# Kernel tuning notes

Measured on AMD Instinct MI355X. Metric: run time of the kernel, lower is better.

## Reference

```python
import jax, jax.numpy as jnp
import numpy as np

ALPHA = 0.1
EPS = 1e-10

def setup_inputs() -> dict:
    key = jax.random.key(0)
    k1, k2 = jax.random.split(key)
    x = jax.random.normal(k1, (64, 8192, 128), dtype=jnp.float32)   # [B, N, D]
    pv = jax.random.uniform(k2, (64, 128), dtype=jnp.float32)        # [M, D] prototypes (torch.rand init)
    return {"x": x, "pv": pv}

def _cdist(x, pv):
    # Euclidean pairwise distance via GEMM form: [B,N,D] x [M,D] -> [B,N,M]
    x2 = jnp.sum(x * x, axis=-1, keepdims=True)          # [B,N,1]
    p2 = jnp.sum(pv * pv, axis=-1)                        # [M]
    xp = jnp.einsum('bnd,md->bnm', x, pv)                 # [B,N,M]
    return jnp.sqrt(jnp.maximum(x2 + p2 - 2.0 * xp, 0.0))

def reference(x, pv):
    dist = _cdist(x, pv)                                  # [B,N,M]
    min_dist = jnp.min(dist, axis=1)                      # [B,M] closest patch per prototype
    min_pos = jnp.argmin(dist, axis=1)                    # [B,M]
    # pick, per batch, the patch position of the globally closest prototype (no-grad in original)
    idx = jnp.argmin(min_dist, axis=1)                    # [B]
    min_pos = min_pos[jnp.arange(min_pos.shape[0]), idx]  # [B]
    max_sim = jnp.exp(EPS - ALPHA * min_dist)             # [B,M]
    return (max_sim, min_pos)
```

## Files before the change

kernel.cpp:

```cpp
#include <hip/hip_runtime.h>
#include <cfloat>
#include <cmath>

#define B_ 64
#define N_ 8192
#define D_ 128
#define M_ 64
#define ROWS 256
#define KD 32
#define NKD (D_ / KD)
#define CHUNKS (N_ / ROWS)
#define ALPHA_ 0.1f
#define EPS_ 1e-10f

__global__ __launch_bounds__(256, 2)
void protomin_kernel(const float* __restrict__ x, const float* __restrict__ pv,
                     float* __restrict__ wsv, int* __restrict__ wsa) {
    __shared__ union U {
        float ps[D_][M_];
        struct R { float rv[M_][33]; int ra[M_][33]; } red;
    } u;
    __shared__ float xs[KD][ROWS];
    __shared__ float x2s[ROWS];
    __shared__ float p2s[M_];

    const int tid   = threadIdx.x;
    const int bc    = blockIdx.x;
    const int b     = bc / CHUNKS;
    const int chunk = bc % CHUNKS;
    const int rowbase = chunk * ROWS;

    const int tm8  = tid & 7;
    const int trow = tid >> 3;
    const int m0   = tm8 * 8;
    const int r0   = trow * 8;

#pragma unroll
    for (int p = 0; p < 8; ++p) {
        int li = p * 1024 + tid * 4;
        int m  = li >> 7;
        int d4 = li & 127;
        float4 v = *reinterpret_cast<const float4*>(pv + m * D_ + d4);
        u.ps[d4 + 0][m] = v.x;
        u.ps[d4 + 1][m] = v.y;
        u.ps[d4 + 2][m] = v.z;
        u.ps[d4 + 3][m] = v.w;
    }
    __syncthreads();

    if (tid < M_) {
        float s = 0.f;
#pragma unroll 8
        for (int d = 0; d < D_; ++d) { float v = u.ps[d][tid]; s = fmaf(v, v, s); }
        p2s[tid] = s;
    }

    float acc[8][8];
#pragma unroll
    for (int i = 0; i < 8; ++i)
#pragma unroll
        for (int j = 0; j < 8; ++j) acc[i][j] = 0.f;
    float x2r = 0.f;

    const float* xbase = x + ((size_t)b * N_ + rowbase) * D_;

    for (int kd = 0; kd < NKD; ++kd) {
        __syncthreads();
#pragma unroll
        for (int p = 0; p < 8; ++p) {
            int li = p * 1024 + tid * 4;
            int r  = li >> 5;
            int dd = li & 31;
            float4 v = *reinterpret_cast<const float4*>(
                xbase + (size_t)r * D_ + kd * KD + dd);
            int rb = r >> 3, rj = r & 7;
            float vv[4] = {v.x, v.y, v.z, v.w};
#pragma unroll
            for (int i = 0; i < 4; ++i) {
                int d = dd + i;
                xs[d][(((rb ^ ((d >> 2) & 7)) << 3) | rj)] = vv[i];
            }
        }
        __syncthreads();

        {
            int rb = tid >> 3, rj = tid & 7;
#pragma unroll 8
            for (int d = 0; d < KD; ++d) {
                float v = xs[d][(((rb ^ ((d >> 2) & 7)) << 3) | rj)];
                x2r = fmaf(v, v, x2r);
            }
        }

        const int dbase = kd * KD;
#pragma unroll 4
        for (int d = 0; d < KD; ++d) {
            int sb = ((trow ^ ((d >> 2) & 7)) << 3);
            float4 xa = *reinterpret_cast<const float4*>(&xs[d][sb]);
            float4 xb = *reinterpret_cast<const float4*>(&xs[d][sb + 4]);
            float4 pa = *reinterpret_cast<const float4*>(&u.ps[dbase + d][m0]);
            float4 pb = *reinterpret_cast<const float4*>(&u.ps[dbase + d][m0 + 4]);
            float xv[8] = {xa.x, xa.y, xa.z, xa.w, xb.x, xb.y, xb.z, xb.w};
            float pw[8] = {pa.x, pa.y, pa.z, pa.w, pb.x, pb.y, pb.z, pb.w};
#pragma unroll
            for (int i = 0; i < 8; ++i)
#pragma unroll
                for (int j = 0; j < 8; ++j)
                    acc[i][j] = fmaf(xv[i], pw[j], acc[i][j]);
        }
    }

    __syncthreads();
    x2s[tid] = x2r;
    __syncthreads();

    float4 xa2 = *reinterpret_cast<const float4*>(&x2s[r0]);
    float4 xb2 = *reinterpret_cast<const float4*>(&x2s[r0 + 4]);
    float x2v[8] = {xa2.x, xa2.y, xa2.z, xa2.w, xb2.x, xb2.y, xb2.z, xb2.w};
    float4 p2a = *reinterpret_cast<const float4*>(&p2s[m0]);
    float4 p2b = *reinterpret_cast<const float4*>(&p2s[m0 + 4]);
    float p2v[8] = {p2a.x, p2a.y, p2a.z, p2a.w, p2b.x, p2b.y, p2b.z, p2b.w};

#pragma unroll
    for (int j = 0; j < 8; ++j) {
        float bv = FLT_MAX; int ba = 0;
        float p2j = p2v[j];
#pragma unroll
        for (int i = 0; i < 8; ++i) {
            float d2 = fmaf(-2.f, acc[i][j], x2v[i] + p2j);
            if (d2 < bv) { bv = d2; ba = rowbase + r0 + i; }
        }
        u.red.rv[m0 + j][trow] = bv;
        u.red.ra[m0 + j][trow] = ba;
    }
    __syncthreads();

    if (tid < M_) {
        float bv = FLT_MAX; int ba = 0;
        for (int k = 0; k < 32; ++k) {
            float v = u.red.rv[tid][k];
            if (v < bv) { bv = v; ba = u.red.ra[tid][k]; }
        }
        wsv[(size_t)bc * M_ + tid] = bv;
        wsa[(size_t)bc * M_ + tid] = ba;
    }
}

__global__ void finalize_kernel(const float* __restrict__ wsv,
                                const int* __restrict__ wsa,
                                float* __restrict__ out) {
    const int b = blockIdx.x;
    const int m = threadIdx.x;
    float bv = FLT_MAX; int ba = 0;
    for (int c = 0; c < CHUNKS; ++c) {
        size_t idx = ((size_t)b * CHUNKS + c) * M_ + m;
        float v = wsv[idx];
        if (v < bv) { bv = v; ba = wsa[idx]; }
    }
    float dist = sqrtf(fmaxf(bv, 0.f));
    out[b * M_ + m] = expf(EPS_ - ALPHA_ * dist);

    __shared__ float sv[M_];
    __shared__ int   sa[M_];
    sv[m] = dist; sa[m] = ba;
    __syncthreads();
    if (m == 0) {
        float best = FLT_MAX; int bp = 0;
        for (int k = 0; k < M_; ++k) {
            if (sv[k] < best) { best = sv[k]; bp = sa[k]; }
        }
        out[B_ * M_ + b] = (float)bp;
    }
}

extern "C" void kernel_launch(void* const* d_in, const int* in_sizes, int n_in,
                              void* d_out, int out_size, void* d_ws, size_t ws_size,
                              hipStream_t stream) {
    const float* x  = (const float*)d_in[0];
    const float* pv = (const float*)d_in[1];
    float* out = (float*)d_out;

    float* wsv = (float*)d_ws;
    int*   wsa = (int*)((char*)d_ws + (size_t)B_ * CHUNKS * M_ * sizeof(float));

    hipLaunchKernelGGL(protomin_kernel, dim3(B_ * CHUNKS), dim3(256), 0, stream,
                       x, pv, wsv, wsa);
    hipLaunchKernelGGL(finalize_kernel, dim3(B_), dim3(M_), 0, stream,
                       wsv, wsa, out);
}
```

Baseline: 438.4 us.

## Rewrite distance GEMM with split-bf16 MFMA and double-buffered register prefetch

```diff
diff --git a/kernel.cpp b/kernel.cpp
--- a/kernel.cpp
+++ b/kernel.cpp
@@ -6,170 +6,210 @@
 #define N_ 8192
 #define D_ 128
 #define M_ 64
-#define ROWS 256
-#define KD 32
-#define NKD (D_ / KD)
-#define CHUNKS (N_ / ROWS)
+#define CROWS 64
+#define NCHUNK 4
+#define BROWS (CROWS*NCHUNK)
+#define NBLK (N_/BROWS)
 #define ALPHA_ 0.1f
 #define EPS_ 1e-10f
 
+typedef __attribute__((ext_vector_type(4))) float f32x4;
+typedef __attribute__((ext_vector_type(8))) short bf16x8;
+typedef __attribute__((ext_vector_type(4))) short s16x4;
+
+static __device__ __forceinline__ short f2bf(float f) {
+    unsigned u = __float_as_uint(f);
+    u += 0x7fff + ((u >> 16) & 1);
+    return (short)(u >> 16);
+}
+static __device__ __forceinline__ float bf2f(short s) {
+    return __uint_as_float(((unsigned)(unsigned short)s) << 16);
+}
+
 __global__ __launch_bounds__(256, 2)
-void protomin_kernel(const float* __restrict__ x, const float* __restrict__ pv,
-                     float* __restrict__ wsv, int* __restrict__ wsa) {
-    __shared__ union U {
-        float ps[D_][M_];
-        struct R { float rv[M_][33]; int ra[M_][33]; } red;
-    } u;
-    __shared__ float xs[KD][ROWS];
-    __shared__ float x2s[ROWS];
-    __shared__ float p2s[M_];
-
-    const int tid   = threadIdx.x;
-    const int bc    = blockIdx.x;
-    const int b     = bc / CHUNKS;
-    const int chunk = bc % CHUNKS;
-    const int rowbase = chunk * ROWS;
-
-    const int tm8  = tid & 7;
-    const int trow = tid >> 3;
-    const int m0   = tm8 * 8;
-    const int r0   = trow * 8;
-
-#pragma unroll
-    for (int p = 0; p < 8; ++p) {
-        int li = p * 1024 + tid * 4;
-        int m  = li >> 7;
-        int d4 = li & 127;
-        float4 v = *reinterpret_cast<const float4*>(pv + m * D_ + d4);
-        u.ps[d4 + 0][m] = v.x;
-        u.ps[d4 + 1][m] = v.y;
-        u.ps[d4 + 2][m] = v.z;
-        u.ps[d4 + 3][m] = v.w;
-    }
+void protomin_mfma(const float* __restrict__ x, const float* __restrict__ pv,
+                   float* __restrict__ wsv, int* __restrict__ wsa) {
+    __shared__ short xhi[2][CROWS * D_];
+    __shared__ short xlo[2][CROWS * D_];
+    __shared__ float x2s[2][CROWS];
+    __shared__ float redv[4][M_];
+    __shared__ int   redp[4][M_];
+
+    const int tid = threadIdx.x;
+    const int w   = tid >> 6;
+    const int l   = tid & 63;
+    const int lm  = l & 15, lg = l >> 4;
+    const int bid = blockIdx.x;
+    const int b   = bid >> 5;
+    const int nbase = (bid & 31) * BROWS;
+
+    const float* xblk = x + ((size_t)b * N_ + nbase) * D_;
+
+    f32x4 nv[8];
+    {
+        const f32x4* src = (const f32x4*)xblk;
+#pragma unroll
+        for (int i = 0; i < 8; ++i) nv[i] = src[(w * 8 + i) * 64 + l];
+    }
+
+    bf16x8 Bh[4][4], Bl[4][4];
+#pragma unroll
+    for (int mt = 0; mt < 4; ++mt) {
+#pragma unroll
+        for (int kt = 0; kt < 4; ++kt) {
+            const float* p = pv + (mt * 16 + lm) * D_ + kt * 32 + lg * 8;
+            f32x4 p0 = *(const f32x4*)p;
+            f32x4 p1 = *(const f32x4*)(p + 4);
+#pragma unroll
+            for (int j = 0; j < 4; ++j) {
+                short h = f2bf(p0[j]);
+                Bh[mt][kt][j] = h;
+                Bl[mt][kt][j] = f2bf(p0[j] - bf2f(h));
+            }
+#pragma unroll
+            for (int j = 0; j < 4; ++j) {
+                short h = f2bf(p1[j]);
+                Bh[mt][kt][4 + j] = h;
+                Bl[mt][kt][4 + j] = f2bf(p1[j] - bf2f(h));
+            }
+        }
+    }
+
+    auto stage = [&](int buf) {
+#pragma unroll
+        for (int i = 0; i < 8; ++i) {
+            int seg = w * 8 + i;
+            int row = seg * 2 + (l >> 5);
+            int ks  = (l & 31) * 4;
+            f32x4 v = nv[i];
+            float s = v[0] * v[0];
+            s = fmaf(v[1], v[1], s); s = fmaf(v[2], v[2], s); s = fmaf(v[3], v[3], s);
+            s += __shfl_xor(s, 1);  s += __shfl_xor(s, 2);  s += __shfl_xor(s, 4);
+            s += __shfl_xor(s, 8);  s += __shfl_xor(s, 16);
+            if ((l & 31) == 0) x2s[buf][row] = s;
+            s16x4 hv, lv;
+#pragma unroll
+            for (int j = 0; j < 4; ++j) {
+                short h = f2bf(v[j]);
+                hv[j] = h;
+                lv[j] = f2bf(v[j] - bf2f(h));
+            }
+            int sidx = row * D_ + (ks ^ ((row & 7) << 3));
+            *(s16x4*)&xhi[buf][sidx] = hv;
+            *(s16x4*)&xlo[buf][sidx] = lv;
+        }
+    };
+
+    float bv[4]; int bp[4];
+#pragma unroll
+    for (int mt = 0; mt < 4; ++mt) { bv[mt] = FLT_MAX; bp[mt] = 0; }
+
+    stage(0);
     __syncthreads();
 
+    for (int c = 0; c < NCHUNK; ++c) {
+        const int cur = c & 1;
+        if (c + 1 < NCHUNK) {
+            const f32x4* src = (const f32x4*)(xblk + (size_t)(c + 1) * CROWS * D_);
+#pragma unroll
+            for (int i = 0; i < 8; ++i) nv[i] = src[(w * 8 + i) * 64 + l];
+        }
+
+        f32x4 acc[4] = {};
+        const int arow  = w * 16 + lm;
+        const int abase = arow * D_;
+        const int aswz  = (arow & 7) << 3;
+#pragma unroll
+        for (int kt = 0; kt < 4; ++kt) {
+            int koff = (kt * 32 + lg * 8) ^ aswz;
+            bf16x8 ah = *(const bf16x8*)&xhi[cur][abase + koff];
+            bf16x8 al = *(const bf16x8*)&xlo[cur][abase + koff];
+#pragma unroll
+            for (int mt = 0; mt < 4; ++mt) {
+                acc[mt] = __builtin_amdgcn_mfma_f32_16x16x32_bf16(ah, Bh[mt][kt], acc[mt], 0, 0, 0);
+                acc[mt] = __builtin_amdgcn_mfma_f32_16x16x32_bf16(al, Bh[mt][kt], acc[mt], 0, 0, 0);
+                acc[mt] = __builtin_amdgcn_mfma_f32_16x16x32_bf16(ah, Bl[mt][kt], acc[mt], 0, 0, 0);
+                acc[mt] = __builtin_amdgcn_mfma_f32_16x16x32_bf16(al, Bl[mt][kt], acc[mt], 0, 0, 0);
+            }
+        }
+
+        float x2v[4];
+        const int rbase = w * 16 + lg * 4;
+#pragma unroll
+        for (int r = 0; r < 4; ++r) x2v[r] = x2s[cur][rbase + r];
+        const int npos0 = nbase + c * CROWS + rbase;
+#pragma unroll
+        for (int mt = 0; mt < 4; ++mt) {
+#pragma unroll
+            for (int r = 0; r < 4; ++r) {
+                float cand = fmaf(-2.f, acc[mt][r], x2v[r]);
+                if (cand < bv[mt]) { bv[mt] = cand; bp[mt] = npos0 + r; }
+            }
+        }
+
+        if (c + 1 < NCHUNK) stage(cur ^ 1);
+        __syncthreads();
+    }
+
+#pragma unroll
+    for (int mt = 0; mt < 4; ++mt) {
+        float v = bv[mt]; int p = bp[mt];
+#pragma unroll
+        for (int off = 16; off <= 32; off <<= 1) {
+            float ov = __shfl_xor(v, off);
+            int   op = __shfl_xor(p, off);
+            if (ov < v || (ov == v && op < p)) { v = ov; p = op; }
+        }
+        if (l < 16) { redv[w][mt * 16 + l] = v; redp[w][mt * 16 + l] = p; }
+    }
+    __syncthreads();
+
     if (tid < M_) {
-        float s = 0.f;
-#pragma unroll 8
-        for (int d = 0; d < D_; ++d) { float v = u.ps[d][tid]; s = fmaf(v, v, s); }
-        p2s[tid] = s;
-    }
-
-    float acc[8][8];
-#pragma unroll
-    for (int i = 0; i < 8; ++i)
-#pragma unroll
-        for (int j = 0; j < 8; ++j) acc[i][j] = 0.f;
-    float x2r = 0.f;
-
-    const float* xbase = x + ((size_t)b * N_ + rowbase) * D_;
-
-    for (int kd = 0; kd < NKD; ++kd) {
-        __syncthreads();
-#pragma unroll
-        for (int p = 0; p < 8; ++p) {
-            int li = p * 1024 + tid * 4;
-            int r  = li >> 5;
-            int dd = li & 31;
-            float4 v = *reinterpret_cast<const float4*>(
-                xbase + (size_t)r * D_ + kd * KD + dd);
-            int rb = r >> 3, rj = r & 7;
-            float vv[4] = {v.x, v.y, v.z, v.w};
-#pragma unroll
-            for (int i = 0; i < 4; ++i) {
-                int d = dd + i;
-                xs[d][(((rb ^ ((d >> 2) & 7)) << 3) | rj)] = vv[i];
-            }
-        }
-        __syncthreads();
-
-        {
-            int rb = tid >> 3, rj = tid & 7;
-#pragma unroll 8
-            for (int d = 0; d < KD; ++d) {
-                float v = xs[d][(((rb ^ ((d >> 2) & 7)) << 3) | rj)];
-                x2r = fmaf(v, v, x2r);
-            }
-        }
-
-        const int dbase = kd * KD;
-#pragma unroll 4
-        for (int d = 0; d < KD; ++d) {
-            int sb = ((trow ^ ((d >> 2) & 7)) << 3);
-            float4 xa = *reinterpret_cast<const float4*>(&xs[d][sb]);
-            float4 xb = *reinterpret_cast<const float4*>(&xs[d][sb + 4]);
-            float4 pa = *reinterpret_cast<const float4*>(&u.ps[dbase + d][m0]);
-            float4 pb = *reinterpret_cast<const float4*>(&u.ps[dbase + d][m0 + 4]);
-            float xv[8] = {xa.x, xa.y, xa.z, xa.w, xb.x, xb.y, xb.z, xb.w};
-            float pw[8] = {pa.x, pa.y, pa.z, pa.w, pb.x, pb.y, pb.z, pb.w};
-#pragma unroll
-            for (int i = 0; i < 8; ++i)
-#pragma unroll
-                for (int j = 0; j < 8; ++j)
-                    acc[i][j] = fmaf(xv[i], pw[j], acc[i][j]);
-        }
-    }
-
-    __syncthreads();
-    x2s[tid] = x2r;
-    __syncthreads();
-
-    float4 xa2 = *reinterpret_cast<const float4*>(&x2s[r0]);
-    float4 xb2 = *reinterpret_cast<const float4*>(&x2s[r0 + 4]);
-    float x2v[8] = {xa2.x, xa2.y, xa2.z, xa2.w, xb2.x, xb2.y, xb2.z, xb2.w};
-    float4 p2a = *reinterpret_cast<const float4*>(&p2s[m0]);
-    float4 p2b = *reinterpret_cast<const float4*>(&p2s[m0 + 4]);
-    float p2v[8] = {p2a.x, p2a.y, p2a.z, p2a.w, p2b.x, p2b.y, p2b.z, p2b.w};
-
-#pragma unroll
-    for (int j = 0; j < 8; ++j) {
-        float bv = FLT_MAX; int ba = 0;
-        float p2j = p2v[j];
-#pragma unroll
-        for (int i = 0; i < 8; ++i) {
-            float d2 = fmaf(-2.f, acc[i][j], x2v[i] + p2j);
-            if (d2 < bv) { bv = d2; ba = rowbase + r0 + i; }
-        }
-        u.red.rv[m0 + j][trow] = bv;
-        u.red.ra[m0 + j][trow] = ba;
-    }
-    __syncthreads();
-
-    if (tid < M_) {
-        float bv = FLT_MAX; int ba = 0;
-        for (int k = 0; k < 32; ++k) {
-            float v = u.red.rv[tid][k];
-            if (v < bv) { bv = v; ba = u.red.ra[tid][k]; }
-        }
-        wsv[(size_t)bc * M_ + tid] = bv;
-        wsa[(size_t)bc * M_ + tid] = ba;
+        float v = redv[0][tid]; int p = redp[0][tid];
+#pragma unroll
+        for (int w2 = 1; w2 < 4; ++w2) {
+            float ov = redv[w2][tid]; int op = redp[w2][tid];
+            if (ov < v || (ov == v && op < p)) { v = ov; p = op; }
+        }
+        wsv[(size_t)bid * M_ + tid] = v;
+        wsa[(size_t)bid * M_ + tid] = p;
     }
 }
 
 __global__ void finalize_kernel(const float* __restrict__ wsv,
                                 const int* __restrict__ wsa,
+                                const float* __restrict__ pv,
                                 float* __restrict__ out) {
     const int b = blockIdx.x;
     const int m = threadIdx.x;
-    float bv = FLT_MAX; int ba = 0;
-    for (int c = 0; c < CHUNKS; ++c) {
-        size_t idx = ((size_t)b * CHUNKS + c) * M_ + m;
-        float v = wsv[idx];
-        if (v < bv) { bv = v; ba = wsa[idx]; }
-    }
-    float dist = sqrtf(fmaxf(bv, 0.f));
+
+    float p2 = 0.f;
+    const f32x4* pp = (const f32x4*)(pv + m * D_);
+#pragma unroll 8
+    for (int j = 0; j < 32; ++j) {
+        f32x4 v = pp[j];
+        p2 = fmaf(v[0], v[0], p2); p2 = fmaf(v[1], v[1], p2);
+        p2 = fmaf(v[2], v[2], p2); p2 = fmaf(v[3], v[3], p2);
+    }
+
+    float v = FLT_MAX; int p = 0;
+    for (int bc = 0; bc < NBLK; ++bc) {
+        size_t idx = ((size_t)(b * NBLK + bc)) * M_ + m;
+        float nv2 = wsv[idx]; int np = wsa[idx];
+        if (nv2 < v || (nv2 == v && np < p)) { v = nv2; p = np; }
+    }
+    float dist = sqrtf(fmaxf(v + p2, 0.f));
     out[b * M_ + m] = expf(EPS_ - ALPHA_ * dist);
 
     __shared__ float sv[M_];
     __shared__ int   sa[M_];
-    sv[m] = dist; sa[m] = ba;
+    sv[m] = dist; sa[m] = p;
     __syncthreads();
     if (m == 0) {
-        float best = FLT_MAX; int bp = 0;
-        for (int k = 0; k < M_; ++k) {
-            if (sv[k] < best) { best = sv[k]; bp = sa[k]; }
-        }
-        out[B_ * M_ + b] = (float)bp;
+        float best = FLT_MAX; int bpos = 0;
+        for (int k = 0; k < M_; ++k)
+            if (sv[k] < best) { best = sv[k]; bpos = sa[k]; }
+        out[B_ * M_ + b] = (float)bpos;
     }
 }
 
@@ -181,10 +221,10 @@
     float* out = (float*)d_out;
 
     float* wsv = (float*)d_ws;
-    int*   wsa = (int*)((char*)d_ws + (size_t)B_ * CHUNKS * M_ * sizeof(float));
-
-    hipLaunchKernelGGL(protomin_kernel, dim3(B_ * CHUNKS), dim3(256), 0, stream,
+    int*   wsa = (int*)((char*)d_ws + (size_t)B_ * NBLK * M_ * sizeof(float));
+
+    hipLaunchKernelGGL(protomin_mfma, dim3(B_ * NBLK), dim3(256), 0, stream,
                        x, pv, wsv, wsa);
     hipLaunchKernelGGL(finalize_kernel, dim3(B_), dim3(M_), 0, stream,
-                       wsv, wsa, out);
-}
+                       wsv, wsa, pv, out);
+}
```

New measurement: 449.5 us. +2.5%, slower.
